# Kernel optimization log

Hardware: AMD Instinct MI355X
Metric: run time of the kernel (lower is better)

## Reference

```python
import jax, jax.numpy as jnp
import numpy as np

HIDDEN = 1024
HEADS = 16
HEAD_DIM = HIDDEN // HEADS  # 64
LOCAL = (128, 128)
ROPE_MAX_POS = LOCAL[0] + LOCAL[1]  # 256 (local attention branch)
ROPE_BASE = 10000.0


def make_rope_cache(max_len, dim, base):
    positions = jnp.arange(max_len, dtype=jnp.float32)
    theta = 1.0 / base ** (jnp.arange(0, dim, 2, dtype=jnp.float32) / dim)
    angles = jnp.einsum('i,j->ij', positions, theta)
    return jnp.stack([jnp.cos(angles), jnp.sin(angles)], axis=-1)  # (max_len, dim//2, 2)


def apply_rope(x, cache):
    # x: (B, S, H, D); cache: (max_pos, D//2, 2)
    S = x.shape[1]
    pos = jnp.arange(S) % cache.shape[0]
    rc = cache[pos][None, :, None, :, :]  # (1, S, 1, D//2, 2)
    xr = x.reshape(*x.shape[:-1], -1, 2)
    x0, x1 = xr[..., 0], xr[..., 1]
    c, s = rc[..., 0], rc[..., 1]
    out = jnp.stack([x0 * c - x1 * s, x1 * c + x0 * s], axis=-1)
    return out.reshape(x.shape)


def sliding_window_mask(S, window, dtype):
    rel = jnp.arange(S)[:, None] - jnp.arange(S)[None, :]
    inside = (rel >= -window[0]) & (rel <= window[1])
    return jnp.where(inside, jnp.zeros((), dtype), -jnp.inf)[None, None]  # (1,1,S,S)


def setup_inputs() -> dict:
    key = jax.random.key(0)
    k1, k2, k3, k4, k5 = jax.random.split(key, 5)
    B, S = 2, 2048
    hidden_states = jax.random.normal(k1, (B, S, HIDDEN), dtype=jnp.float32)
    Wqkv_kernel = jax.random.normal(k2, (HIDDEN, 3 * HIDDEN), dtype=jnp.float32) / np.sqrt(HIDDEN)
    Wqkv_bias = jnp.zeros((3 * HIDDEN,), dtype=jnp.float32)
    Wo_kernel = jax.random.normal(k3, (HIDDEN, HIDDEN), dtype=jnp.float32) / np.sqrt(HIDDEN)
    Wo_bias = jnp.zeros((HIDDEN,), dtype=jnp.float32)
    rope_cache = make_rope_cache(ROPE_MAX_POS, HEAD_DIM, ROPE_BASE)
    return {
        'hidden_states': hidden_states,
        'Wqkv_kernel': Wqkv_kernel,
        'Wqkv_bias': Wqkv_bias,
        'Wo_kernel': Wo_kernel,
        'Wo_bias': Wo_bias,
        'rope_cache': rope_cache,
    }


def reference(hidden_states, Wqkv_kernel, Wqkv_bias, Wo_kernel, Wo_bias, rope_cache):
    B, S, _ = hidden_states.shape
    qkv = hidden_states @ Wqkv_kernel + Wqkv_bias  # (B,S,3*HIDDEN)
    qkv = qkv.reshape(B, S, 3, HEADS, HEAD_DIM)
    q = qkv[:, :, 0]  # (B,S,H,D)
    k = qkv[:, :, 1]
    v = qkv[:, :, 2]
    q = apply_rope(q, rope_cache)
    k = apply_rope(k, rope_cache)
    # to (B,H,S,D)
    q = jnp.transpose(q, (0, 2, 1, 3))
    k = jnp.transpose(k, (0, 2, 1, 3))
    v = jnp.transpose(v, (0, 2, 1, 3))
    scale = jnp.sqrt(jnp.float32(HEAD_DIM))
    scores = jnp.einsum('bhqd,bhkd->bhqk', q, k) / scale
    mask = sliding_window_mask(S, LOCAL, scores.dtype)
    probs = jax.nn.softmax(scores + mask, axis=-1)
    out = jnp.einsum('bhqk,bhkd->bqhd', probs, v).reshape(B, S, HIDDEN)
    out = out @ Wo_kernel + Wo_bias
    return out
```

## Files before the change

### kernel.cpp

```cpp
#include <hip/hip_runtime.h>
#include <hip/hip_bf16.h>

typedef __bf16 bf16x8 __attribute__((ext_vector_type(8)));
typedef __bf16 bf16x4 __attribute__((ext_vector_type(4)));
typedef float f32x4 __attribute__((ext_vector_type(4)));

#define SLEN 2048
#define NHEADS 16
#define HDIM 64

__device__ __forceinline__ void async_copy16(const __bf16* g, void* l) {
    __builtin_amdgcn_global_load_lds(
        (const __attribute__((address_space(1))) void*)g,
        (__attribute__((address_space(3))) void*)l, 16, 0, 0);
}

__global__ __launch_bounds__(256) void cast_f32_bf16(const float* __restrict__ in,
                                                     __bf16* __restrict__ out, int n4) {
    int i = blockIdx.x * 256 + threadIdx.x;
    if (i < n4) {
        float4 v = reinterpret_cast<const float4*>(in)[i];
        bf16x4 o = { (__bf16)v.x, (__bf16)v.y, (__bf16)v.z, (__bf16)v.w };
        reinterpret_cast<bf16x4*>(out)[i] = o;
    }
}

__global__ __launch_bounds__(256) void transpose_cast(const float* __restrict__ W,
                                                      __bf16* __restrict__ Wt,
                                                      int K, int N) {
    __shared__ float tile[32][33];
    int n0 = blockIdx.x * 32, k0 = blockIdx.y * 32;
    int tx = threadIdx.x, ty = threadIdx.y;
    #pragma unroll
    for (int i = ty; i < 32; i += 8)
        tile[i][tx] = W[(size_t)(k0 + i) * N + n0 + tx];
    __syncthreads();
    #pragma unroll
    for (int i = ty; i < 32; i += 8)
        Wt[(size_t)(n0 + i) * K + k0 + tx] = (__bf16)tile[tx][i];
}

__global__ __launch_bounds__(256) void gemm_bt(const __bf16* __restrict__ A,
                                               const __bf16* __restrict__ Bt,
                                               const float* __restrict__ bias,
                                               const float* __restrict__ rope,
                                               float* __restrict__ Cf,
                                               __bf16* __restrict__ Cq,
                                               __bf16* __restrict__ Ck,
                                               __bf16* __restrict__ Cv,
                                               int M, int N, int K, int epi) {
    __shared__ __align__(16) __bf16 As[128 * 32];
    __shared__ __align__(16) __bf16 Bs[128 * 32];

    int nb = N >> 7;
    int bx = blockIdx.x % nb;
    int by = blockIdx.x / nb;
    int row0 = by * 128, col0 = bx * 128;

    int tid = threadIdx.x;
    int wave = tid >> 6, lane = tid & 63;
    int quad = lane >> 4, lrow = lane & 15;
    int wm = wave >> 1, wn = wave & 1;

    int r1 = tid >> 2;
    int kk = (tid & 3) * 8;
    int kg = kk ^ (((r1 >> 1) & 3) * 8);
    const __bf16* Ap = A + (size_t)(row0 + r1) * K + kg;
    const __bf16* Bp = Bt + (size_t)(col0 + r1) * K + kg;
    char* as_lo = (char*)As + wave * 1024;
    char* bs_lo = (char*)Bs + wave * 1024;

    f32x4 acc[4][4];
    f32x4 zero = {0.f, 0.f, 0.f, 0.f};
    #pragma unroll
    for (int i = 0; i < 4; i++)
        #pragma unroll
        for (int j = 0; j < 4; j++) acc[i][j] = zero;

    int sA = (quad ^ ((lrow >> 1) & 3)) * 8;

    for (int k0 = 0; k0 < K; k0 += 32) {
        __syncthreads();
        async_copy16(Ap + k0, as_lo);
        async_copy16(Ap + (size_t)64 * K + k0, as_lo + 4096);
        async_copy16(Bp + k0, bs_lo);
        async_copy16(Bp + (size_t)64 * K + k0, bs_lo + 4096);
        __syncthreads();

        bf16x8 af[4], bfr[4];
        #pragma unroll
        for (int i = 0; i < 4; i++)
            af[i] = *reinterpret_cast<const bf16x8*>(&As[(wm * 64 + i * 16 + lrow) * 32 + sA]);
        #pragma unroll
        for (int j = 0; j < 4; j++)
            bfr[j] = *reinterpret_cast<const bf16x8*>(&Bs[(wn * 64 + j * 16 + lrow) * 32 + sA]);
        #pragma unroll
        for (int i = 0; i < 4; i++)
            #pragma unroll
            for (int j = 0; j < 4; j++)
                acc[i][j] = __builtin_amdgcn_mfma_f32_16x16x32_bf16(af[i], bfr[j], acc[i][j], 0, 0, 0);
    }

    int part = col0 >> 10;
    bool do_rope = (epi == 1) && (part < 2);
    #pragma unroll
    for (int i = 0; i < 4; i++) {
        int rowb = row0 + wm * 64 + i * 16 + quad * 4;
        #pragma unroll
        for (int j = 0; j < 4; j++) {
            int col = col0 + wn * 64 + j * 16 + lrow;
            float bsv = bias[col];
            int d = col & 63;
            #pragma unroll
            for (int r = 0; r < 4; r++) {
                int row = rowb + r;
                float v = acc[i][j][r] + bsv;
                if (do_rope) {
                    int pos = row & 255;
                    int p = d >> 1;
                    float c  = rope[(pos * 32 + p) * 2];
                    float sn = rope[(pos * 32 + p) * 2 + 1];
                    float other = __shfl_xor(v, 1, 64);
                    v = (d & 1) ? fmaf(v, c, other * sn) : fmaf(v, c, -other * sn);
                }
                if (epi == 0) {
                    Cf[(size_t)row * N + col] = v;
                } else {
                    int h = (col >> 6) & 15;
                    int b = row >> 11;
                    int s = row & 2047;
                    __bf16* dst = (part == 0) ? Cq : ((part == 1) ? Ck : Cv);
                    dst[((size_t)(b * NHEADS + h) * SLEN + s) * HDIM + d] = (__bf16)v;
                }
            }
        }
    }
}

__global__ __launch_bounds__(256) void attn_kernel(const __bf16* __restrict__ Q,
                                                   const __bf16* __restrict__ Kt,
                                                   const __bf16* __restrict__ V,
                                                   __bf16* __restrict__ O) {
    __shared__ __align__(16) __bf16 Vt[64][72];
    __shared__ __align__(16) __bf16 Pl[4][16][72];

    int qt = blockIdx.x & 31;
    int bh = blockIdx.x >> 5;
    int q0 = qt * 64;
    const __bf16* Qbh = Q + (size_t)bh * SLEN * HDIM;
    const __bf16* Kbh = Kt + (size_t)bh * SLEN * HDIM;
    const __bf16* Vbh = V + (size_t)bh * SLEN * HDIM;

    int tid = threadIdx.x;
    int wave = tid >> 6, lane = tid & 63;
    int quad = lane >> 4, lrow = lane & 15;
    int wq0 = q0 + wave * 16;

    bf16x8 qa0 = *reinterpret_cast<const bf16x8*>(Qbh + (size_t)(wq0 + lrow) * HDIM + quad * 8);
    bf16x8 qa1 = *reinterpret_cast<const bf16x8*>(Qbh + (size_t)(wq0 + lrow) * HDIM + 32 + quad * 8);

    f32x4 zero = {0.f, 0.f, 0.f, 0.f};
    f32x4 acc[4];
    #pragma unroll
    for (int t = 0; t < 4; t++) acc[t] = zero;
    float m_i[4], l_i[4];
    #pragma unroll
    for (int r = 0; r < 4; r++) { m_i[r] = -1e30f; l_i[r] = 0.f; }

    int kstart = q0 - 128; if (kstart < 0) kstart = 0;
    int kend = q0 + 63 + 128 + 1; if (kend > SLEN) kend = SLEN;

    for (int kc = kstart; kc < kend; kc += 64) {
        __syncthreads();
        {
            int keyl = tid >> 2;
            int db = (tid & 3) * 16;
            const __bf16* vp = Vbh + (size_t)(kc + keyl) * HDIM + db;
            bf16x8 v0 = *reinterpret_cast<const bf16x8*>(vp);
            bf16x8 v1 = *reinterpret_cast<const bf16x8*>(vp + 8);
            #pragma unroll
            for (int i = 0; i < 8; i++) {
                Vt[db + i][keyl] = v0[i];
                Vt[db + 8 + i][keyl] = v1[i];
            }
        }
        __syncthreads();

        f32x4 cs[4];
        #pragma unroll
        for (int sub = 0; sub < 4; sub++) {
            cs[sub] = zero;
            const __bf16* krow = Kbh + (size_t)(kc + sub * 16 + lrow) * HDIM;
            bf16x8 kba = *reinterpret_cast<const bf16x8*>(krow + quad * 8);
            bf16x8 kbb = *reinterpret_cast<const bf16x8*>(krow + 32 + quad * 8);
            cs[sub] = __builtin_amdgcn_mfma_f32_16x16x32_bf16(qa0, kba, cs[sub], 0, 0, 0);
            cs[sub] = __builtin_amdgcn_mfma_f32_16x16x32_bf16(qa1, kbb, cs[sub], 0, 0, 0);
        }

        #pragma unroll
        for (int r = 0; r < 4; r++) {
            int q = wq0 + quad * 4 + r;
            float sc[4];
            bool vd[4];
            #pragma unroll
            for (int sub = 0; sub < 4; sub++) {
                int key = kc + sub * 16 + lrow;
                vd[sub] = (key >= q - 128) && (key <= q + 128);
                sc[sub] = vd[sub] ? cs[sub][r] * 0.125f : -1e30f;
            }
            float rm = fmaxf(fmaxf(sc[0], sc[1]), fmaxf(sc[2], sc[3]));
            #pragma unroll
            for (int off = 1; off < 16; off <<= 1) rm = fmaxf(rm, __shfl_xor(rm, off, 64));
            float mnew = fmaxf(m_i[r], rm);
            float alpha = __expf(m_i[r] - mnew);
            float p[4], rs = 0.f;
            #pragma unroll
            for (int sub = 0; sub < 4; sub++) {
                p[sub] = vd[sub] ? __expf(sc[sub] - mnew) : 0.0f;
                rs += p[sub];
            }
            #pragma unroll
            for (int off = 1; off < 16; off <<= 1) rs += __shfl_xor(rs, off, 64);
            l_i[r] = l_i[r] * alpha + rs;
            m_i[r] = mnew;
            #pragma unroll
            for (int t = 0; t < 4; t++) acc[t][r] *= alpha;
            #pragma unroll
            for (int sub = 0; sub < 4; sub++)
                Pl[wave][quad * 4 + r][sub * 16 + lrow] = (__bf16)p[sub];
        }
        asm volatile("s_waitcnt lgkmcnt(0)" ::: "memory");

        bf16x8 ap0 = *reinterpret_cast<const bf16x8*>(&Pl[wave][lrow][quad * 8]);
        bf16x8 ap1 = *reinterpret_cast<const bf16x8*>(&Pl[wave][lrow][32 + quad * 8]);
        #pragma unroll
        for (int t = 0; t < 4; t++) {
            bf16x8 bv0 = *reinterpret_cast<const bf16x8*>(&Vt[t * 16 + lrow][quad * 8]);
            bf16x8 bv1 = *reinterpret_cast<const bf16x8*>(&Vt[t * 16 + lrow][32 + quad * 8]);
            acc[t] = __builtin_amdgcn_mfma_f32_16x16x32_bf16(ap0, bv0, acc[t], 0, 0, 0);
            acc[t] = __builtin_amdgcn_mfma_f32_16x16x32_bf16(ap1, bv1, acc[t], 0, 0, 0);
        }
    }

    int b = bh >> 4, h = bh & 15;
    #pragma unroll
    for (int r = 0; r < 4; r++) {
        int stok = q0 + wave * 16 + quad * 4 + r;
        float inv = 1.0f / l_i[r];
        size_t base = ((size_t)b * SLEN + stok) * 1024 + h * HDIM;
        #pragma unroll
        for (int t = 0; t < 4; t++) {
            O[base + t * 16 + lrow] = (__bf16)(acc[t][r] * inv);
        }
    }
}

extern "C" void kernel_launch(void* const* d_in, const int* in_sizes, int n_in,
                              void* d_out, int out_size, void* d_ws, size_t ws_size,
                              hipStream_t stream) {
    const float* hidden = (const float*)d_in[0];
    const float* Wqkv   = (const float*)d_in[1];
    const float* bqkv   = (const float*)d_in[2];
    const float* Wo     = (const float*)d_in[3];
    const float* bo     = (const float*)d_in[4];
    const float* rope   = (const float*)d_in[5];
    float* out = (float*)d_out;

    char* ws = (char*)d_ws;
    __bf16* A1  = (__bf16*)(ws);
    __bf16* Wt  = (__bf16*)(ws + 8388608);
    __bf16* Wot = (__bf16*)(ws + 14680064);
    __bf16* Qb  = (__bf16*)(ws + 16777216);
    __bf16* Kb  = (__bf16*)(ws + 25165824);
    __bf16* Vb  = (__bf16*)(ws + 33554432);
    __bf16* AO  = (__bf16*)(ws + 41943040);

    cast_f32_bf16<<<4096, 256, 0, stream>>>(hidden, A1, 1048576);
    transpose_cast<<<dim3(96, 32), dim3(32, 8), 0, stream>>>(Wqkv, Wt, 1024, 3072);
    transpose_cast<<<dim3(32, 32), dim3(32, 8), 0, stream>>>(Wo, Wot, 1024, 1024);

    gemm_bt<<<32 * 24, 256, 0, stream>>>(A1, Wt, bqkv, rope, nullptr, Qb, Kb, Vb,
                                         4096, 3072, 1024, 1);
    attn_kernel<<<2 * 16 * 32, 256, 0, stream>>>(Qb, Kb, Vb, AO);
    gemm_bt<<<32 * 8, 256, 0, stream>>>(AO, Wot, bo, rope, out, nullptr, nullptr, nullptr,
                                        4096, 1024, 1024, 0);
}
```

Measured before the change: 207.5 us.

## Restructure sliding-window attention and retile output GEMM with register-staged loads

Result: faster. 201.0 us (-3.1%).

```diff
diff --git a/kernel.cpp b/kernel.cpp
--- a/kernel.cpp
+++ b/kernel.cpp
@@ -8,12 +8,6 @@
 #define SLEN 2048
 #define NHEADS 16
 #define HDIM 64
-
-__device__ __forceinline__ void async_copy16(const __bf16* g, void* l) {
-    __builtin_amdgcn_global_load_lds(
-        (const __attribute__((address_space(1))) void*)g,
-        (__attribute__((address_space(3))) void*)l, 16, 0, 0);
-}
 
 __global__ __launch_bounds__(256) void cast_f32_bf16(const float* __restrict__ in,
                                                      __bf16* __restrict__ out, int n4) {
@@ -40,6 +34,7 @@
         Wt[(size_t)(n0 + i) * K + k0 + tx] = (__bf16)tile[tx][i];
 }
 
+template <int TN>
 __global__ __launch_bounds__(256) void gemm_bt(const __bf16* __restrict__ A,
                                                const __bf16* __restrict__ Bt,
                                                const float* __restrict__ bias,
@@ -49,13 +44,14 @@
                                                __bf16* __restrict__ Ck,
                                                __bf16* __restrict__ Cv,
                                                int M, int N, int K, int epi) {
+    constexpr int JN = TN / 32;
     __shared__ __align__(16) __bf16 As[128 * 32];
-    __shared__ __align__(16) __bf16 Bs[128 * 32];
-
-    int nb = N >> 7;
+    __shared__ __align__(16) __bf16 Bs[TN * 32];
+
+    int nb = N / TN;
     int bx = blockIdx.x % nb;
     int by = blockIdx.x / nb;
-    int row0 = by * 128, col0 = bx * 128;
+    int row0 = by * 128, col0 = bx * TN;
 
     int tid = threadIdx.x;
     int wave = tid >> 6, lane = tid & 63;
@@ -67,37 +63,40 @@
     int kg = kk ^ (((r1 >> 1) & 3) * 8);
     const __bf16* Ap = A + (size_t)(row0 + r1) * K + kg;
     const __bf16* Bp = Bt + (size_t)(col0 + r1) * K + kg;
-    char* as_lo = (char*)As + wave * 1024;
-    char* bs_lo = (char*)Bs + wave * 1024;
-
-    f32x4 acc[4][4];
+
+    f32x4 acc[4][JN];
     f32x4 zero = {0.f, 0.f, 0.f, 0.f};
     #pragma unroll
     for (int i = 0; i < 4; i++)
         #pragma unroll
-        for (int j = 0; j < 4; j++) acc[i][j] = zero;
+        for (int j = 0; j < JN; j++) acc[i][j] = zero;
 
     int sA = (quad ^ ((lrow >> 1) & 3)) * 8;
 
     for (int k0 = 0; k0 < K; k0 += 32) {
+        bf16x8 a0 = *reinterpret_cast<const bf16x8*>(Ap + k0);
+        bf16x8 a1 = *reinterpret_cast<const bf16x8*>(Ap + (size_t)64 * K + k0);
+        bf16x8 b0 = *reinterpret_cast<const bf16x8*>(Bp + k0);
+        bf16x8 b1;
+        if (TN == 128) b1 = *reinterpret_cast<const bf16x8*>(Bp + (size_t)64 * K + k0);
         __syncthreads();
-        async_copy16(Ap + k0, as_lo);
-        async_copy16(Ap + (size_t)64 * K + k0, as_lo + 4096);
-        async_copy16(Bp + k0, bs_lo);
-        async_copy16(Bp + (size_t)64 * K + k0, bs_lo + 4096);
+        *reinterpret_cast<bf16x8*>(&As[r1 * 32 + kk]) = a0;
+        *reinterpret_cast<bf16x8*>(&As[(r1 + 64) * 32 + kk]) = a1;
+        *reinterpret_cast<bf16x8*>(&Bs[r1 * 32 + kk]) = b0;
+        if (TN == 128) *reinterpret_cast<bf16x8*>(&Bs[(r1 + 64) * 32 + kk]) = b1;
         __syncthreads();
 
-        bf16x8 af[4], bfr[4];
+        bf16x8 af[4], bfr[JN];
         #pragma unroll
         for (int i = 0; i < 4; i++)
             af[i] = *reinterpret_cast<const bf16x8*>(&As[(wm * 64 + i * 16 + lrow) * 32 + sA]);
         #pragma unroll
-        for (int j = 0; j < 4; j++)
-            bfr[j] = *reinterpret_cast<const bf16x8*>(&Bs[(wn * 64 + j * 16 + lrow) * 32 + sA]);
+        for (int j = 0; j < JN; j++)
+            bfr[j] = *reinterpret_cast<const bf16x8*>(&Bs[(wn * (TN / 2) + j * 16 + lrow) * 32 + sA]);
         #pragma unroll
         for (int i = 0; i < 4; i++)
             #pragma unroll
-            for (int j = 0; j < 4; j++)
+            for (int j = 0; j < JN; j++)
                 acc[i][j] = __builtin_amdgcn_mfma_f32_16x16x32_bf16(af[i], bfr[j], acc[i][j], 0, 0, 0);
     }
 
@@ -107,8 +106,8 @@
     for (int i = 0; i < 4; i++) {
         int rowb = row0 + wm * 64 + i * 16 + quad * 4;
         #pragma unroll
-        for (int j = 0; j < 4; j++) {
-            int col = col0 + wn * 64 + j * 16 + lrow;
+        for (int j = 0; j < JN; j++) {
+            int col = col0 + wn * (TN / 2) + j * 16 + lrow;
             float bsv = bias[col];
             int d = col & 63;
             #pragma unroll
@@ -138,17 +137,18 @@
 }
 
 __global__ __launch_bounds__(256) void attn_kernel(const __bf16* __restrict__ Q,
-                                                   const __bf16* __restrict__ Kt,
+                                                   const __bf16* __restrict__ K,
                                                    const __bf16* __restrict__ V,
                                                    __bf16* __restrict__ O) {
-    __shared__ __align__(16) __bf16 Vt[64][72];
-    __shared__ __align__(16) __bf16 Pl[4][16][72];
+    __shared__ __align__(16) __bf16 Vt[64][328];
+    __shared__ __align__(16) __bf16 Pl[4][16][40];
 
     int qt = blockIdx.x & 31;
     int bh = blockIdx.x >> 5;
     int q0 = qt * 64;
+    int kbase0 = q0 - 128;
     const __bf16* Qbh = Q + (size_t)bh * SLEN * HDIM;
-    const __bf16* Kbh = Kt + (size_t)bh * SLEN * HDIM;
+    const __bf16* Kbh = K + (size_t)bh * SLEN * HDIM;
     const __bf16* Vbh = V + (size_t)bh * SLEN * HDIM;
 
     int tid = threadIdx.x;
@@ -156,102 +156,93 @@
     int quad = lane >> 4, lrow = lane & 15;
     int wq0 = q0 + wave * 16;
 
-    bf16x8 qa0 = *reinterpret_cast<const bf16x8*>(Qbh + (size_t)(wq0 + lrow) * HDIM + quad * 8);
-    bf16x8 qa1 = *reinterpret_cast<const bf16x8*>(Qbh + (size_t)(wq0 + lrow) * HDIM + 32 + quad * 8);
-
-    f32x4 zero = {0.f, 0.f, 0.f, 0.f};
-    f32x4 acc[4];
-    #pragma unroll
-    for (int t = 0; t < 4; t++) acc[t] = zero;
-    float m_i[4], l_i[4];
-    #pragma unroll
-    for (int r = 0; r < 4; r++) { m_i[r] = -1e30f; l_i[r] = 0.f; }
-
-    int kstart = q0 - 128; if (kstart < 0) kstart = 0;
-    int kend = q0 + 63 + 128 + 1; if (kend > SLEN) kend = SLEN;
-
-    for (int kc = kstart; kc < kend; kc += 64) {
-        __syncthreads();
-        {
-            int keyl = tid >> 2;
-            int db = (tid & 3) * 16;
-            const __bf16* vp = Vbh + (size_t)(kc + keyl) * HDIM + db;
+    {
+        int dchunk = wave * 16;
+        #pragma unroll
+        for (int k = 0; k < 5; k++) {
+            int off = k * 64 + lane;
+            int krow = kbase0 + off;
+            krow = min(max(krow, 0), SLEN - 1);
+            const __bf16* vp = Vbh + (size_t)krow * HDIM + dchunk;
             bf16x8 v0 = *reinterpret_cast<const bf16x8*>(vp);
             bf16x8 v1 = *reinterpret_cast<const bf16x8*>(vp + 8);
             #pragma unroll
             for (int i = 0; i < 8; i++) {
-                Vt[db + i][keyl] = v0[i];
-                Vt[db + 8 + i][keyl] = v1[i];
+                Vt[dchunk + i][off] = v0[i];
+                Vt[dchunk + 8 + i][off] = v1[i];
             }
         }
-        __syncthreads();
-
-        f32x4 cs[4];
-        #pragma unroll
-        for (int sub = 0; sub < 4; sub++) {
-            cs[sub] = zero;
-            const __bf16* krow = Kbh + (size_t)(kc + sub * 16 + lrow) * HDIM;
-            bf16x8 kba = *reinterpret_cast<const bf16x8*>(krow + quad * 8);
-            bf16x8 kbb = *reinterpret_cast<const bf16x8*>(krow + 32 + quad * 8);
-            cs[sub] = __builtin_amdgcn_mfma_f32_16x16x32_bf16(qa0, kba, cs[sub], 0, 0, 0);
-            cs[sub] = __builtin_amdgcn_mfma_f32_16x16x32_bf16(qa1, kbb, cs[sub], 0, 0, 0);
-        }
-
-        #pragma unroll
-        for (int r = 0; r < 4; r++) {
-            int q = wq0 + quad * 4 + r;
-            float sc[4];
-            bool vd[4];
-            #pragma unroll
-            for (int sub = 0; sub < 4; sub++) {
-                int key = kc + sub * 16 + lrow;
-                vd[sub] = (key >= q - 128) && (key <= q + 128);
-                sc[sub] = vd[sub] ? cs[sub][r] * 0.125f : -1e30f;
+    }
+
+    bf16x8 qb0 = *reinterpret_cast<const bf16x8*>(Qbh + (size_t)(wq0 + lrow) * HDIM + quad * 8);
+    bf16x8 qb1 = *reinterpret_cast<const bf16x8*>(Qbh + (size_t)(wq0 + lrow) * HDIM + 32 + quad * 8);
+
+    __syncthreads();
+
+    f32x4 zero = {0.f, 0.f, 0.f, 0.f};
+    f32x4 acc[4], acc_l = zero;
+    #pragma unroll
+    for (int t = 0; t < 4; t++) acc[t] = zero;
+
+    bf16x8 ones = { (__bf16)1.f, (__bf16)1.f, (__bf16)1.f, (__bf16)1.f,
+                    (__bf16)1.f, (__bf16)1.f, (__bf16)1.f, (__bf16)1.f };
+
+    int cbeg = wave >> 1;
+    if (q0 < 128) { int e = (128 - q0) >> 5; if (e > cbeg) cbeg = e; }
+    int cend = (16 * wave + 271) >> 5;
+    { int e = (2175 - q0) >> 5; if (e < cend) cend = e; }
+
+    for (int c = cbeg; c <= cend; c++) {
+        int kb = kbase0 + c * 32;
+        int loc = c * 32;
+
+        f32x4 st[2];
+        #pragma unroll
+        for (int sub = 0; sub < 2; sub++) {
+            int kr = kb + sub * 16 + lrow;
+            int krc = min(max(kr, 0), SLEN - 1);
+            const __bf16* kp = Kbh + (size_t)krc * HDIM;
+            bf16x8 ka0 = *reinterpret_cast<const bf16x8*>(kp + quad * 8);
+            bf16x8 ka1 = *reinterpret_cast<const bf16x8*>(kp + 32 + quad * 8);
+            st[sub] = __builtin_amdgcn_mfma_f32_16x16x32_bf16(ka0, qb0, zero, 0, 0, 0);
+            st[sub] = __builtin_amdgcn_mfma_f32_16x16x32_bf16(ka1, qb1, st[sub], 0, 0, 0);
+        }
+
+        int q = wq0 + lrow;
+        #pragma unroll
+        for (int sub = 0; sub < 2; sub++) {
+            bf16x4 pk;
+            #pragma unroll
+            for (int r = 0; r < 4; r++) {
+                int key = kb + sub * 16 + quad * 4 + r;
+                int rel = key - q;
+                bool valid = (rel >= -128) && (rel <= 128) && (key >= 0) && (key < SLEN);
+                float p = valid ? __expf(st[sub][r] * 0.125f) : 0.0f;
+                pk[r] = (__bf16)p;
             }
-            float rm = fmaxf(fmaxf(sc[0], sc[1]), fmaxf(sc[2], sc[3]));
-            #pragma unroll
-            for (int off = 1; off < 16; off <<= 1) rm = fmaxf(rm, __shfl_xor(rm, off, 64));
-            float mnew = fmaxf(m_i[r], rm);
-            float alpha = __expf(m_i[r] - mnew);
-            float p[4], rs = 0.f;
-            #pragma unroll
-            for (int sub = 0; sub < 4; sub++) {
-                p[sub] = vd[sub] ? __expf(sc[sub] - mnew) : 0.0f;
-                rs += p[sub];
-            }
-            #pragma unroll
-            for (int off = 1; off < 16; off <<= 1) rs += __shfl_xor(rs, off, 64);
-            l_i[r] = l_i[r] * alpha + rs;
-            m_i[r] = mnew;
-            #pragma unroll
-            for (int t = 0; t < 4; t++) acc[t][r] *= alpha;
-            #pragma unroll
-            for (int sub = 0; sub < 4; sub++)
-                Pl[wave][quad * 4 + r][sub * 16 + lrow] = (__bf16)p[sub];
+            *reinterpret_cast<bf16x4*>(&Pl[wave][lrow][sub * 16 + quad * 4]) = pk;
         }
         asm volatile("s_waitcnt lgkmcnt(0)" ::: "memory");
 
-        bf16x8 ap0 = *reinterpret_cast<const bf16x8*>(&Pl[wave][lrow][quad * 8]);
-        bf16x8 ap1 = *reinterpret_cast<const bf16x8*>(&Pl[wave][lrow][32 + quad * 8]);
+        bf16x8 bp = *reinterpret_cast<const bf16x8*>(&Pl[wave][lrow][quad * 8]);
+        acc_l = __builtin_amdgcn_mfma_f32_16x16x32_bf16(ones, bp, acc_l, 0, 0, 0);
         #pragma unroll
         for (int t = 0; t < 4; t++) {
-            bf16x8 bv0 = *reinterpret_cast<const bf16x8*>(&Vt[t * 16 + lrow][quad * 8]);
-            bf16x8 bv1 = *reinterpret_cast<const bf16x8*>(&Vt[t * 16 + lrow][32 + quad * 8]);
-            acc[t] = __builtin_amdgcn_mfma_f32_16x16x32_bf16(ap0, bv0, acc[t], 0, 0, 0);
-            acc[t] = __builtin_amdgcn_mfma_f32_16x16x32_bf16(ap1, bv1, acc[t], 0, 0, 0);
-        }
-    }
-
+            bf16x8 va = *reinterpret_cast<const bf16x8*>(&Vt[t * 16 + lrow][loc + quad * 8]);
+            acc[t] = __builtin_amdgcn_mfma_f32_16x16x32_bf16(va, bp, acc[t], 0, 0, 0);
+        }
+    }
+
+    float inv = 1.0f / acc_l[0];
     int b = bh >> 4, h = bh & 15;
-    #pragma unroll
-    for (int r = 0; r < 4; r++) {
-        int stok = q0 + wave * 16 + quad * 4 + r;
-        float inv = 1.0f / l_i[r];
-        size_t base = ((size_t)b * SLEN + stok) * 1024 + h * HDIM;
-        #pragma unroll
-        for (int t = 0; t < 4; t++) {
-            O[base + t * 16 + lrow] = (__bf16)(acc[t][r] * inv);
-        }
+    int q = wq0 + lrow;
+    size_t base = ((size_t)b * SLEN + q) * 1024 + h * HDIM;
+    #pragma unroll
+    for (int t = 0; t < 4; t++) {
+        bf16x4 o;
+        #pragma unroll
+        for (int r = 0; r < 4; r++) o[r] = (__bf16)(acc[t][r] * inv);
+        *reinterpret_cast<bf16x4*>(&O[base + t * 16 + quad * 4]) = o;
     }
 }
 
@@ -279,9 +270,9 @@
     transpose_cast<<<dim3(96, 32), dim3(32, 8), 0, stream>>>(Wqkv, Wt, 1024, 3072);
     transpose_cast<<<dim3(32, 32), dim3(32, 8), 0, stream>>>(Wo, Wot, 1024, 1024);
 
-    gemm_bt<<<32 * 24, 256, 0, stream>>>(A1, Wt, bqkv, rope, nullptr, Qb, Kb, Vb,
-                                         4096, 3072, 1024, 1);
-    attn_kernel<<<2 * 16 * 32, 256, 0, stream>>>(Qb, Kb, Vb, AO);
-    gemm_bt<<<32 * 8, 256, 0, stream>>>(AO, Wot, bo, rope, out, nullptr, nullptr, nullptr,
-                                        4096, 1024, 1024, 0);
-}
+    gemm_bt<128><<<32 * 24, 256, 0, stream>>>(A1, Wt, bqkv, rope, nullptr, Qb, Kb, Vb,
+                                              4096, 3072, 1024, 1);
+    attn_kernel<<<1024, 256, 0, stream>>>(Qb, Kb, Vb, AO);
+    gemm_bt<64><<<32 * 16, 256, 0, stream>>>(AO, Wot, bo, rope, out, nullptr, nullptr, nullptr,
+                                             4096, 1024, 1024, 0);
+}
```
